# Kernel tuning notes

Measured on AMD Instinct MI355X. Metric: run time of the kernel, lower is better.

## Reference

```python
import jax, jax.numpy as jnp
import numpy as np
import math

C = 91                      # num classes incl. background
BBOX_CLIP = math.log(1000.0 / 16.0)
IMG_H, IMG_W = 800.0, 800.0
SCORE_THRESH = 0.05
NMS_THRESH = 0.5
DETS_PER_IMG = 100
MIN_SIZE = 0.01
WX, WY, WW, WH = 10.0, 10.0, 5.0, 5.0   # bbox_reg_weights


def setup_inputs() -> dict:
    key = jax.random.key(0)
    ks = jax.random.split(key, 8)
    B, N, F_IN, HID = 4, 2048, 12544, 1024
    box_features = jax.random.normal(ks[0], (B, N, F_IN), jnp.float32) * 0.1
    # valid proposal boxes inside an 800x800 image: x1y1 in [0,600], wh in [10,200]
    xy = jax.random.uniform(ks[1], (B, N, 2), jnp.float32, minval=0.0, maxval=600.0)
    wh = jax.random.uniform(ks[2], (B, N, 2), jnp.float32, minval=10.0, maxval=200.0)
    proposals = jnp.concatenate([xy, xy + wh], axis=-1)
    def sc(k, sh, fan):
        return jax.random.normal(k, sh, jnp.float32) * (1.0 / np.sqrt(fan))
    return {
        'box_features': box_features,
        'proposals': proposals,
        'fc6_w': sc(ks[3], (F_IN, HID), F_IN), 'fc6_b': jnp.zeros((HID,), jnp.float32),
        'fc7_w': sc(ks[4], (HID, HID), HID),   'fc7_b': jnp.zeros((HID,), jnp.float32),
        'cls_w': sc(ks[5], (HID, C), HID),     'cls_b': jnp.zeros((C,), jnp.float32),
        'bbox_w': sc(ks[6], (HID, 4 * C), HID), 'bbox_b': jnp.zeros((4 * C,), jnp.float32),
    }


def decode_boxes(rel, props):
    w = props[:, 2] - props[:, 0]
    h = props[:, 3] - props[:, 1]
    cx = props[:, 0] + 0.5 * w
    cy = props[:, 1] + 0.5 * h
    dx = rel[..., 0] / WX
    dy = rel[..., 1] / WY
    dw = jnp.minimum(rel[..., 2] / WW, BBOX_CLIP)
    dh = jnp.minimum(rel[..., 3] / WH, BBOX_CLIP)
    pcx = dx * w[:, None] + cx[:, None]
    pcy = dy * h[:, None] + cy[:, None]
    pw = jnp.exp(dw) * w[:, None]
    ph = jnp.exp(dh) * h[:, None]
    return jnp.stack([pcx - 0.5 * pw, pcy - 0.5 * ph,
                      pcx + 0.5 * pw, pcy + 0.5 * ph], axis=-1)


def postprocess_one(logits, regr, props):
    # logits [N,C], regr [N,4C], props [N,4] -> padded top-DETS_PER_IMG detections
    N = logits.shape[0]
    boxes = decode_boxes(regr.reshape(N, C, 4), props)        # [N,C,4]
    scores = jax.nn.softmax(logits, axis=-1)                  # [N,C]
    # clip_boxes_to_image
    x = jnp.clip(boxes[..., 0::2], 0.0, IMG_W)
    y = jnp.clip(boxes[..., 1::2], 0.0, IMG_H)
    boxes = jnp.stack([x[..., 0], y[..., 0], x[..., 1], y[..., 1]], axis=-1)
    # drop background class, flatten candidates
    boxes = boxes[:, 1:].reshape(-1, 4)                       # [M,4], M=N*(C-1)
    scores = scores[:, 1:].reshape(-1)                        # [M]
    labels = jnp.broadcast_to(jnp.arange(1, C, dtype=jnp.int32)[None, :],
                              (N, C - 1)).reshape(-1)         # [M]
    # score threshold + remove_small_boxes (invalidate instead of dynamic gather)
    bw = boxes[:, 2] - boxes[:, 0]
    bh = boxes[:, 3] - boxes[:, 1]
    valid = (scores > SCORE_THRESH) & (bw >= MIN_SIZE) & (bh >= MIN_SIZE)
    s0 = jnp.where(valid, scores, -jnp.inf)
    # batched_nms via per-class coordinate offset
    offset = labels.astype(boxes.dtype)[:, None] * (max(IMG_H, IMG_W) + 1.0)
    ob = boxes + offset
    area = (ob[:, 2] - ob[:, 0]) * (ob[:, 3] - ob[:, 1])

    def body(sc_cur, _):
        best = jnp.argmax(sc_cur)
        bb = ob[best]
        lt = jnp.maximum(ob[:, :2], bb[:2])
        rb = jnp.minimum(ob[:, 2:], bb[2:])
        inter = jnp.prod(jnp.maximum(rb - lt, 0.0), axis=-1)
        union = jnp.maximum(area + area[best] - inter, 1e-6)
        iou = inter / union
        sc_new = jnp.where(iou > NMS_THRESH, -jnp.inf, sc_cur)
        return sc_new, (best, sc_cur[best])

    _, (keep, kept_s) = jax.lax.scan(body, s0, None, length=DETS_PER_IMG)
    ok = jnp.isfinite(kept_s)
    out_boxes = jnp.where(ok[:, None], boxes[keep], 0.0)      # [D,4]
    out_scores = jnp.where(ok, kept_s, 0.0)                   # [D]
    out_labels = jnp.where(ok, labels[keep], 0)               # [D] int32
    return out_boxes, out_scores, out_labels


def reference(box_features, proposals, fc6_w, fc6_b, fc7_w, fc7_b,
              cls_w, cls_b, bbox_w, bbox_b):
    # TwoMLPHead
    h = jax.nn.relu(box_features @ fc6_w + fc6_b)             # [B,N,1024]
    h = jax.nn.relu(h @ fc7_w + fc7_b)
    # FastRCNNPredictor
    logits = h @ cls_w + cls_b                                # [B,N,C]
    regr = h @ bbox_w + bbox_b                                # [B,N,4C]
    boxes, scores, labels = jax.vmap(postprocess_one)(logits, regr, proposals)
    return boxes, scores, labels
```

## Files before the change

### kernel.cpp

```cpp
#include <hip/hip_runtime.h>
#include <math.h>

#define NIMG   4
#define NPROP  2048
#define MTOT   8192
#define FIN    12544
#define HID    1024
#define NC     91
#define NCB    512
#define DETS   100
#define CAPMAX (NPROP * (NC - 1))
#define VLDS   6144

typedef __attribute__((ext_vector_type(8))) short short8;
typedef __attribute__((ext_vector_type(4))) float f32x4;

__device__ __forceinline__ unsigned short f2bf(float f) {
  union { float f; unsigned u; } v; v.f = f;
  unsigned r = v.u + 0x7fffu + ((v.u >> 16) & 1u);
  return (unsigned short)(r >> 16);
}

__device__ __forceinline__ unsigned cvtpk(float lo, float hi) {
  unsigned r;
  asm("v_cvt_pk_bf16_f32 %0, %1, %2" : "=v"(r) : "v"(lo), "v"(hi));
  return r;
}

__device__ __forceinline__ void gload_lds16(const void* g, void* l) {
  __builtin_amdgcn_global_load_lds((__attribute__((address_space(1))) void*)(g),
                                   (__attribute__((address_space(3))) void*)(l), 16, 0, 0);
}

__global__ void transpose_cvt(const float* __restrict__ in, unsigned short* __restrict__ out,
                              int K, int N, int row_off, int out_ld) {
  __shared__ float tile[32][33];
  int k0 = blockIdx.y * 32, n0 = blockIdx.x * 32;
  int tx = threadIdx.x, ty = threadIdx.y;
#pragma unroll
  for (int i = 0; i < 4; ++i) {
    int r = ty + i * 8;
    if (k0 + r < K && n0 + tx < N)
      tile[r][tx] = in[(size_t)(k0 + r) * N + (n0 + tx)];
  }
  __syncthreads();
#pragma unroll
  for (int i = 0; i < 4; ++i) {
    int r = ty + i * 8;
    if (n0 + r < N && k0 + tx < K)
      out[(size_t)(row_off + n0 + r) * out_ld + (k0 + tx)] = f2bf(tile[tx][r]);
  }
}

__global__ void prep_misc(unsigned short* __restrict__ Wcbt, float* __restrict__ bias_cb,
                          const float* __restrict__ cls_b, const float* __restrict__ bbox_b,
                          int* __restrict__ ccount) {
  int i = blockIdx.x * blockDim.x + threadIdx.x;
  int stride = gridDim.x * blockDim.x;
  for (int j = i; j < 57 * 1024; j += stride) Wcbt[455 * 1024 + j] = 0;
  for (int j = i; j < NCB; j += stride)
    bias_cb[j] = (j < 91) ? cls_b[j] : ((j < 455) ? bbox_b[j - 91] : 0.0f);
  if (i < NIMG) ccount[i] = 0;
}

template <bool AFP32, bool RELU, bool OUTBF16>
__global__ __launch_bounds__(512, 2) void gemm_nt(const void* __restrict__ Av,
                                                  const unsigned short* __restrict__ Bt,
                                                  const float* __restrict__ bias,
                                                  void* __restrict__ Cv,
                                                  int M, int N, int K) {
  __shared__ __align__(16) unsigned short As[2][256 * 64];
  __shared__ __align__(16) unsigned short Bs[2][128 * 64];
  const int tid  = threadIdx.x;
  const int lane = tid & 63;
  const int wid  = tid >> 6;
  const int wm   = (wid >> 1) * 64;
  const int wn   = (wid & 1) * 64;
  const int m0   = blockIdx.x * 256, n0 = blockIdx.y * 128;
  const int lcol = lane & 15;
  const int lk4  = lane >> 4;
  const int rsw  = lcol & 7;

  const int st_r  = lane >> 3;
  const int st_kc = ((lane & 7) ^ st_r) << 3;

  f32x4 acc[4][4];
#pragma unroll
  for (int a = 0; a < 4; ++a)
#pragma unroll
    for (int b = 0; b < 4; ++b)
#pragma unroll
      for (int r = 0; r < 4; ++r) acc[a][b][r] = 0.0f;

  const int NT = K >> 6;
  float4 pa[4][2];

  auto stage_async = [&](int buf, int t) {
    const int k0 = t << 6;
#pragma unroll
    for (int i = 0; i < 2; ++i) {
      int chunk = (wid << 1) | i;
      int r = (chunk << 3) | st_r;
      gload_lds16(Bt + (size_t)(n0 + r) * K + k0 + st_kc, &Bs[buf][chunk << 9]);
    }
    if constexpr (!AFP32) {
#pragma unroll
      for (int i = 0; i < 4; ++i) {
        int chunk = (wid << 2) | i;
        int r = (chunk << 3) | st_r;
        gload_lds16((const unsigned short*)Av + (size_t)(m0 + r) * K + k0 + st_kc,
                    &As[buf][chunk << 9]);
      }
    }
  };
  auto loadA = [&](int t) {
    const int k0 = t << 6;
#pragma unroll
    for (int i = 0; i < 4; ++i) {
      int s = tid + (i << 9);
      int row = s >> 3, kc = (s & 7) << 3;
      const float* gp = (const float*)Av + (size_t)(m0 + row) * K + (k0 + kc);
      pa[i][0] = *(const float4*)gp;
      pa[i][1] = *(const float4*)(gp + 4);
    }
  };
  auto writeA = [&](int buf) {
#pragma unroll
    for (int i = 0; i < 4; ++i) {
      int s = tid + (i << 9);
      int row = s >> 3;
      int slot = ((s & 7) ^ (row & 7)) << 3;
      union { unsigned u32[4]; short8 s8; } pk;
      pk.u32[0] = cvtpk(pa[i][0].x, pa[i][0].y);
      pk.u32[1] = cvtpk(pa[i][0].z, pa[i][0].w);
      pk.u32[2] = cvtpk(pa[i][1].x, pa[i][1].y);
      pk.u32[3] = cvtpk(pa[i][1].z, pa[i][1].w);
      *(short8*)&As[buf][row * 64 + slot] = pk.s8;
    }
  };

  stage_async(0, 0);
  if constexpr (AFP32) { loadA(0); writeA(0); }
  __syncthreads();

  int cur = 0;
  for (int t = 0; t < NT; ++t) {
    const int nxt = cur ^ 1;
    if (t + 1 < NT) {
      stage_async(nxt, t + 1);
      if constexpr (AFP32) loadA(t + 1);
    }
#pragma unroll
    for (int kk = 0; kk < 2; ++kk) {
      const int sb = kk << 2;
      short8 af[4], bf[4];
#pragma unroll
      for (int im = 0; im < 4; ++im)
        af[im] = *(const short8*)&As[cur][(wm + im * 16 + lcol) * 64 + (((sb + lk4) ^ rsw) << 3)];
#pragma unroll
      for (int in = 0; in < 4; ++in)
        bf[in] = *(const short8*)&Bs[cur][(wn + in * 16 + lcol) * 64 + (((sb + lk4) ^ rsw) << 3)];
      __builtin_amdgcn_s_setprio(1);
#pragma unroll
      for (int im = 0; im < 4; ++im)
#pragma unroll
        for (int in = 0; in < 4; ++in)
          acc[im][in] = __builtin_amdgcn_mfma_f32_16x16x32_bf16(af[im], bf[in], acc[im][in], 0, 0, 0);
      __builtin_amdgcn_s_setprio(0);
    }
    if (t + 1 < NT) { if constexpr (AFP32) writeA(nxt); }
    __syncthreads();
    cur = nxt;
  }

  const int r0 = (lane >> 4) * 4;
#pragma unroll
  for (int im = 0; im < 4; ++im) {
#pragma unroll
    for (int in = 0; in < 4; ++in) {
      int gn = n0 + wn + in * 16 + lcol;
      float bv = bias[gn];
#pragma unroll
      for (int r = 0; r < 4; ++r) {
        int gm = m0 + wm + im * 16 + r0 + r;
        float vv = acc[im][in][r] + bv;
        if (RELU) vv = fmaxf(vv, 0.0f);
        if (OUTBF16) ((unsigned short*)Cv)[(size_t)gm * N + gn] = f2bf(vv);
        else         ((float*)Cv)[(size_t)gm * N + gn] = vv;
      }
    }
  }
}

__global__ void candgen(const float* __restrict__ out3, const float* __restrict__ props,
                        float* __restrict__ cscore, float* __restrict__ cbox,
                        int* __restrict__ clabel, int* __restrict__ ccount, int CAP) {
  int gw   = (blockIdx.x * blockDim.x + threadIdx.x) >> 6;
  int lane = threadIdx.x & 63;
  if (gw >= MTOT) return;
  int img = gw >> 11;
  const float* row = out3 + (size_t)gw * NCB;

  float l0 = row[lane];
  float l1 = (lane < NC - 64) ? row[64 + lane] : -INFINITY;
  float mx = fmaxf(l0, l1);
#pragma unroll
  for (int off = 32; off; off >>= 1) mx = fmaxf(mx, __shfl_xor(mx, off));
  float e0 = expf(l0 - mx);
  float e1 = (lane < NC - 64) ? expf(l1 - mx) : 0.0f;
  float den = e0 + e1;
#pragma unroll
  for (int off = 32; off; off >>= 1) den += __shfl_xor(den, off);
  float inv = 1.0f / den;

  float4 p = *(const float4*)(props + (size_t)gw * 4);
  float w = p.z - p.x, h = p.w - p.y;
  float cx = p.x + 0.5f * w, cy = p.y + 0.5f * h;

#pragma unroll
  for (int half = 0; half < 2; ++half) {
    int c = (half << 6) + lane;
    float s = (half ? e1 : e0) * inv;
    if (c >= 1 && c < NC && s > 0.05f) {
      float dx = row[91 + c * 4 + 0] * 0.1f;
      float dy = row[91 + c * 4 + 1] * 0.1f;
      float dw = fminf(row[91 + c * 4 + 2] * 0.2f, 4.135166556742356f);
      float dh = fminf(row[91 + c * 4 + 3] * 0.2f, 4.135166556742356f);
      float pcx = dx * w + cx, pcy = dy * h + cy;
      float pw = expf(dw) * w, ph = expf(dh) * h;
      float x1 = fminf(fmaxf(pcx - 0.5f * pw, 0.0f), 800.0f);
      float x2 = fminf(fmaxf(pcx + 0.5f * pw, 0.0f), 800.0f);
      float y1 = fminf(fmaxf(pcy - 0.5f * ph, 0.0f), 800.0f);
      float y2 = fminf(fmaxf(pcy + 0.5f * ph, 0.0f), 800.0f);
      if (x2 - x1 >= 0.01f && y2 - y1 >= 0.01f) {
        int idx = atomicAdd(&ccount[img], 1);
        if (idx < CAP) {
          size_t o = (size_t)img * CAP + idx;
          cscore[o] = s;
          clabel[o] = c;
          cbox[o * 4 + 0] = x1; cbox[o * 4 + 1] = y1;
          cbox[o * 4 + 2] = x2; cbox[o * 4 + 3] = y2;
        }
      }
    }
  }
}

__global__ __launch_bounds__(1024) void nms_kernel(float* __restrict__ cscore, const float* __restrict__ cbox,
                           const int* __restrict__ clabel, const int* __restrict__ ccount,
                           float* __restrict__ out, int CAP) {
  int img = blockIdx.x;
  int tid = threadIdx.x;
  int lane = tid & 63, wid = tid >> 6;
  int V = ccount[img]; if (V > CAP) V = CAP;
  int VL = V < VLDS ? V : VLDS;
  float* sc = cscore + (size_t)img * CAP;
  const float* bx = cbox + (size_t)img * CAP * 4;
  const int* lb = clabel + (size_t)img * CAP;
  float* ob  = out + (size_t)img * DETS * 4;
  float* osd = out + (size_t)NIMG * DETS * 4 + (size_t)img * DETS;
  float* ol  = out + (size_t)NIMG * DETS * 5 + (size_t)img * DETS;

  for (int t = tid; t < DETS; t += blockDim.x) {
    ob[t * 4 + 0] = 0.0f; ob[t * 4 + 1] = 0.0f; ob[t * 4 + 2] = 0.0f; ob[t * 4 + 3] = 0.0f;
    osd[t] = 0.0f; ol[t] = 0.0f;
  }

  __shared__ float sx1[VLDS], sy1[VLDS], sx2[VLDS], sy2[VLDS], sar[VLDS], ssc[VLDS];
  __shared__ float rs[16]; __shared__ int ri[16];
  __shared__ float bbs[6];
  __shared__ int   bbest;

  for (int t = tid; t < VL; t += blockDim.x) {
    float4 b = *(const float4*)&bx[(size_t)t * 4];
    float offv = (float)lb[t] * 801.0f;
    sx1[t] = b.x + offv; sy1[t] = b.y + offv;
    sx2[t] = b.z + offv; sy2[t] = b.w + offv;
    sar[t] = (b.z - b.x) * (b.w - b.y);
    ssc[t] = sc[t];
  }
  __syncthreads();

  for (int d = 0; d < DETS; ++d) {
    float bs = -INFINITY; int bi = -1;
    for (int t = tid; t < VL; t += blockDim.x) { float v = ssc[t]; if (v > bs) { bs = v; bi = t; } }
    if (V > VLDS)
      for (int t = VLDS + tid; t < V; t += blockDim.x) { float v = sc[t]; if (v > bs) { bs = v; bi = t; } }
#pragma unroll
    for (int off = 32; off; off >>= 1) {
      float osf = __shfl_xor(bs, off); int oi = __shfl_xor(bi, off);
      if (osf > bs) { bs = osf; bi = oi; }
    }
    if (lane == 0) { rs[wid] = bs; ri[wid] = bi; }
    __syncthreads();
    if (tid == 0) {
      float b0 = rs[0]; int i0 = ri[0];
      for (int wv = 1; wv < 16; ++wv) if (rs[wv] > b0) { b0 = rs[wv]; i0 = ri[wv]; }
      if (i0 < 0 || !(b0 > -INFINITY)) {
        bbest = -1;
      } else {
        bbest = i0;
        float ox1, oy1, ox2, oy2, ar;
        if (i0 < VLDS) { ox1 = sx1[i0]; oy1 = sy1[i0]; ox2 = sx2[i0]; oy2 = sy2[i0]; ar = sar[i0]; }
        else {
          float4 b = *(const float4*)&bx[(size_t)i0 * 4];
          float offv = (float)lb[i0] * 801.0f;
          ox1 = b.x + offv; oy1 = b.y + offv; ox2 = b.z + offv; oy2 = b.w + offv;
          ar = (b.z - b.x) * (b.w - b.y);
        }
        bbs[0] = ox1; bbs[1] = oy1; bbs[2] = ox2; bbs[3] = oy2; bbs[4] = ar;
        float4 rb = *(const float4*)&bx[(size_t)i0 * 4];
        ob[d * 4 + 0] = rb.x; ob[d * 4 + 1] = rb.y; ob[d * 4 + 2] = rb.z; ob[d * 4 + 3] = rb.w;
        osd[d] = b0;
        ol[d] = (float)lb[i0];
      }
    }
    __syncthreads();
    if (bbest < 0) break;
    float bx1 = bbs[0], by1 = bbs[1], bx2 = bbs[2], by2 = bbs[3], barea = bbs[4];
    for (int t = tid; t < VL; t += blockDim.x) {
      float ltx = fmaxf(sx1[t], bx1), lty = fmaxf(sy1[t], by1);
      float rbx = fminf(sx2[t], bx2), rby = fminf(sy2[t], by2);
      float inter = fmaxf(rbx - ltx, 0.0f) * fmaxf(rby - lty, 0.0f);
      float uni = fmaxf(sar[t] + barea - inter, 1e-6f);
      if (inter / uni > 0.5f) ssc[t] = -INFINITY;
    }
    if (V > VLDS) {
      for (int t = VLDS + tid; t < V; t += blockDim.x) {
        float4 b = *(const float4*)&bx[(size_t)t * 4];
        float offv = (float)lb[t] * 801.0f;
        float tx1 = b.x + offv, ty1 = b.y + offv, tx2 = b.z + offv, ty2 = b.w + offv;
        float ltx = fmaxf(tx1, bx1), lty = fmaxf(ty1, by1);
        float rbx = fminf(tx2, bx2), rby = fminf(ty2, by2);
        float inter = fmaxf(rbx - ltx, 0.0f) * fmaxf(rby - lty, 0.0f);
        float areat = (tx2 - tx1) * (ty2 - ty1);
        float uni = fmaxf(areat + barea - inter, 1e-6f);
        if (inter / uni > 0.5f) sc[t] = -INFINITY;
      }
    }
    __syncthreads();
  }
}

extern "C" void kernel_launch(void* const* d_in, const int* in_sizes, int n_in,
                              void* d_out, int out_size, void* d_ws, size_t ws_size,
                              hipStream_t stream) {
  const float* box_features = (const float*)d_in[0];
  const float* proposals    = (const float*)d_in[1];
  const float* fc6_w = (const float*)d_in[2];
  const float* fc6_b = (const float*)d_in[3];
  const float* fc7_w = (const float*)d_in[4];
  const float* fc7_b = (const float*)d_in[5];
  const float* cls_w = (const float*)d_in[6];
  const float* cls_b = (const float*)d_in[7];
  const float* bbox_w = (const float*)d_in[8];
  const float* bbox_b = (const float*)d_in[9];

  char* ws = (char*)d_ws;
  size_t off = 0;
  unsigned short* W6t  = (unsigned short*)(ws + off); off += (size_t)HID * FIN * 2;
  unsigned short* W7t  = (unsigned short*)(ws + off); off += (size_t)HID * HID * 2;
  unsigned short* Wcbt = (unsigned short*)(ws + off); off += (size_t)NCB * HID * 2;
  float* bias_cb       = (float*)(ws + off);          off += (size_t)NCB * 4;
  int*   ccount        = (int*)(ws + off);            off += 256;
  unsigned short* h1   = (unsigned short*)(ws + off); off += (size_t)MTOT * HID * 2;
  unsigned short* h2   = (unsigned short*)(ws + off); off += (size_t)MTOT * HID * 2;
  float* out3          = (float*)(ws + off);          off += (size_t)MTOT * NCB * 4;

  int CAP = CAPMAX;
  if (ws_size > off) {
    size_t avail = ws_size - off;
    size_t cap_ws = avail / 96;
    if (cap_ws < (size_t)CAP) CAP = (int)cap_ws;
  } else {
    CAP = 0;
  }
  float* cscore = (float*)(ws + off);
  int*   clabel = (int*)(ws + off + (size_t)NIMG * CAP * 4);
  float* cbox   = (float*)(ws + off + (size_t)NIMG * CAP * 8);

  transpose_cvt<<<dim3(HID / 32, FIN / 32), dim3(32, 8), 0, stream>>>(fc6_w, W6t, FIN, HID, 0, FIN);
  transpose_cvt<<<dim3(HID / 32, HID / 32), dim3(32, 8), 0, stream>>>(fc7_w, W7t, HID, HID, 0, HID);
  transpose_cvt<<<dim3(3,  HID / 32), dim3(32, 8), 0, stream>>>(cls_w,  Wcbt, HID, 91,  0,  HID);
  transpose_cvt<<<dim3(12, HID / 32), dim3(32, 8), 0, stream>>>(bbox_w, Wcbt, HID, 364, 91, HID);
  prep_misc<<<64, 256, 0, stream>>>(Wcbt, bias_cb, cls_b, bbox_b, ccount);

  gemm_nt<true,  true,  true ><<<dim3(MTOT / 256, HID / 128), 512, 0, stream>>>(
      box_features, W6t, fc6_b, h1, MTOT, HID, FIN);
  gemm_nt<false, true,  true ><<<dim3(MTOT / 256, HID / 128), 512, 0, stream>>>(
      h1, W7t, fc7_b, h2, MTOT, HID, HID);
  gemm_nt<false, false, false><<<dim3(MTOT / 256, NCB / 128), 512, 0, stream>>>(
      h2, Wcbt, bias_cb, out3, MTOT, NCB, HID);

  candgen<<<(MTOT * 64) / 256, 256, 0, stream>>>(out3, proposals, cscore, cbox, clabel, ccount, CAP);
  nms_kernel<<<NIMG, 1024, 0, stream>>>(cscore, cbox, clabel, ccount, (float*)d_out, CAP);
}
```

Measured before the change: 991.7 us.

## Reshape GEMM tiles to 128x256 and hand-tune vmcnt waits for prefetch overlap

Each GEMM block now covers 128 rows and 256 columns (128 for the final small GEMM) instead of 256x128. The large fp32 activation matrix in fc6 is therefore re-read across half as many column tiles, which cuts global traffic on the dominant operand. The loop also replaces __syncthreads with explicit s_waitcnt vmcnt counts and raw barriers. This lets the next tile's loads stay in flight while the current tile is computed. In exchange there are fewer accumulators per wave along M, and occupancy and LDS use change. The hand-counted vmcnt values must match the number of loads issued, or correctness breaks.

```diff
diff --git a/kernel.cpp b/kernel.cpp
--- a/kernel.cpp
+++ b/kernel.cpp
@@ -32,6 +32,13 @@
                                    (__attribute__((address_space(3))) void*)(l), 16, 0, 0);
 }
 
+template <int N> __device__ __forceinline__ void waitcnt_vm() {
+  if constexpr (N == 8)      asm volatile("s_waitcnt vmcnt(8)" ::: "memory");
+  else if constexpr (N == 6) asm volatile("s_waitcnt vmcnt(6)" ::: "memory");
+  else if constexpr (N == 4) asm volatile("s_waitcnt vmcnt(4)" ::: "memory");
+  else                       asm volatile("s_waitcnt vmcnt(0)" ::: "memory");
+}
+
 __global__ void transpose_cvt(const float* __restrict__ in, unsigned short* __restrict__ out,
                               int K, int N, int row_off, int out_ld) {
   __shared__ float tile[32][33];
@@ -63,20 +70,24 @@
   if (i < NIMG) ccount[i] = 0;
 }
 
-template <bool AFP32, bool RELU, bool OUTBF16>
-__global__ __launch_bounds__(512, 2) void gemm_nt(const void* __restrict__ Av,
-                                                  const unsigned short* __restrict__ Bt,
-                                                  const float* __restrict__ bias,
-                                                  void* __restrict__ Cv,
-                                                  int M, int N, int K) {
-  __shared__ __align__(16) unsigned short As[2][256 * 64];
-  __shared__ __align__(16) unsigned short Bs[2][128 * 64];
+template <int BN, bool AFP32, bool RELU, bool OUTBF16>
+__global__ __launch_bounds__(512, (BN == 256) ? 2 : 4)
+void gemm_nt(const void* __restrict__ Av, const unsigned short* __restrict__ Bt,
+             const float* __restrict__ bias, void* __restrict__ Cv,
+             int M, int N, int K) {
+  constexpr int WN   = BN / 4;
+  constexpr int NAN_ = WN / 16;
+  constexpr int BCH  = BN / 64;
+  constexpr int VISS = AFP32 ? 8 : (2 + BCH);
+
+  __shared__ __align__(16) unsigned short As[2][128 * 64];
+  __shared__ __align__(16) unsigned short Bs[2][BN * 64];
   const int tid  = threadIdx.x;
   const int lane = tid & 63;
   const int wid  = tid >> 6;
-  const int wm   = (wid >> 1) * 64;
-  const int wn   = (wid & 1) * 64;
-  const int m0   = blockIdx.x * 256, n0 = blockIdx.y * 128;
+  const int wm   = (wid >> 2) * 64;
+  const int wn   = (wid & 3) * WN;
+  const int m0   = blockIdx.x * 128, n0 = blockIdx.y * BN;
   const int lcol = lane & 15;
   const int lk4  = lane >> 4;
   const int rsw  = lcol & 7;
@@ -84,29 +95,29 @@
   const int st_r  = lane >> 3;
   const int st_kc = ((lane & 7) ^ st_r) << 3;
 
-  f32x4 acc[4][4];
+  f32x4 acc[4][NAN_];
 #pragma unroll
   for (int a = 0; a < 4; ++a)
 #pragma unroll
-    for (int b = 0; b < 4; ++b)
+    for (int b = 0; b < NAN_; ++b)
 #pragma unroll
       for (int r = 0; r < 4; ++r) acc[a][b][r] = 0.0f;
 
   const int NT = K >> 6;
-  float4 pa[4][2];
+  float4 pa[2][2];
 
   auto stage_async = [&](int buf, int t) {
     const int k0 = t << 6;
 #pragma unroll
-    for (int i = 0; i < 2; ++i) {
-      int chunk = (wid << 1) | i;
+    for (int i = 0; i < BCH; ++i) {
+      int chunk = wid * BCH + i;
       int r = (chunk << 3) | st_r;
       gload_lds16(Bt + (size_t)(n0 + r) * K + k0 + st_kc, &Bs[buf][chunk << 9]);
     }
     if constexpr (!AFP32) {
 #pragma unroll
-      for (int i = 0; i < 4; ++i) {
-        int chunk = (wid << 2) | i;
+      for (int i = 0; i < 2; ++i) {
+        int chunk = (wid << 1) | i;
         int r = (chunk << 3) | st_r;
         gload_lds16((const unsigned short*)Av + (size_t)(m0 + r) * K + k0 + st_kc,
                     &As[buf][chunk << 9]);
@@ -116,7 +127,7 @@
   auto loadA = [&](int t) {
     const int k0 = t << 6;
 #pragma unroll
-    for (int i = 0; i < 4; ++i) {
+    for (int i = 0; i < 2; ++i) {
       int s = tid + (i << 9);
       int row = s >> 3, kc = (s & 7) << 3;
       const float* gp = (const float*)Av + (size_t)(m0 + row) * K + (k0 + kc);
@@ -126,7 +137,7 @@
   };
   auto writeA = [&](int buf) {
 #pragma unroll
-    for (int i = 0; i < 4; ++i) {
+    for (int i = 0; i < 2; ++i) {
       int s = tid + (i << 9);
       int row = s >> 3;
       int slot = ((s & 7) ^ (row & 7)) << 3;
@@ -139,37 +150,52 @@
     }
   };
 
+  if constexpr (AFP32) loadA(0);
   stage_async(0, 0);
-  if constexpr (AFP32) { loadA(0); writeA(0); }
-  __syncthreads();
+  if constexpr (AFP32) writeA(0);
+  asm volatile("s_waitcnt vmcnt(0) lgkmcnt(0)" ::: "memory");
+  __builtin_amdgcn_s_barrier();
+  __builtin_amdgcn_sched_barrier(0);
 
   int cur = 0;
   for (int t = 0; t < NT; ++t) {
     const int nxt = cur ^ 1;
     if (t + 1 < NT) {
+      if constexpr (AFP32) loadA(t + 1);
       stage_async(nxt, t + 1);
-      if constexpr (AFP32) loadA(t + 1);
-    }
+      waitcnt_vm<VISS>();
+    } else {
+      waitcnt_vm<0>();
+    }
+    __builtin_amdgcn_s_barrier();
+    __builtin_amdgcn_sched_barrier(0);
 #pragma unroll
     for (int kk = 0; kk < 2; ++kk) {
       const int sb = kk << 2;
-      short8 af[4], bf[4];
+      short8 af[4], bf[NAN_];
 #pragma unroll
       for (int im = 0; im < 4; ++im)
         af[im] = *(const short8*)&As[cur][(wm + im * 16 + lcol) * 64 + (((sb + lk4) ^ rsw) << 3)];
 #pragma unroll
-      for (int in = 0; in < 4; ++in)
+      for (int in = 0; in < NAN_; ++in)
         bf[in] = *(const short8*)&Bs[cur][(wn + in * 16 + lcol) * 64 + (((sb + lk4) ^ rsw) << 3)];
       __builtin_amdgcn_s_setprio(1);
 #pragma unroll
       for (int im = 0; im < 4; ++im)
 #pragma unroll
-        for (int in = 0; in < 4; ++in)
+        for (int in = 0; in < NAN_; ++in)
           acc[im][in] = __builtin_amdgcn_mfma_f32_16x16x32_bf16(af[im], bf[in], acc[im][in], 0, 0, 0);
       __builtin_amdgcn_s_setprio(0);
     }
-    if (t + 1 < NT) { if constexpr (AFP32) writeA(nxt); }
-    __syncthreads();
+    if (t + 1 < NT) {
+      if constexpr (AFP32) {
+        writeA(nxt);
+        asm volatile("s_waitcnt lgkmcnt(0)" ::: "memory");
+      }
+    }
+    __builtin_amdgcn_sched_barrier(0);
+    __builtin_amdgcn_s_barrier();
+    __builtin_amdgcn_sched_barrier(0);
     cur = nxt;
   }
 
@@ -177,7 +203,7 @@
 #pragma unroll
   for (int im = 0; im < 4; ++im) {
 #pragma unroll
-    for (int in = 0; in < 4; ++in) {
+    for (int in = 0; in < NAN_; ++in) {
       int gn = n0 + wn + in * 16 + lcol;
       float bv = bias[gn];
 #pragma unroll
@@ -385,11 +411,11 @@
   transpose_cvt<<<dim3(12, HID / 32), dim3(32, 8), 0, stream>>>(bbox_w, Wcbt, HID, 364, 91, HID);
   prep_misc<<<64, 256, 0, stream>>>(Wcbt, bias_cb, cls_b, bbox_b, ccount);
 
-  gemm_nt<true,  true,  true ><<<dim3(MTOT / 256, HID / 128), 512, 0, stream>>>(
+  gemm_nt<256, true,  true,  true ><<<dim3(MTOT / 128, HID / 256), 512, 0, stream>>>(
       box_features, W6t, fc6_b, h1, MTOT, HID, FIN);
-  gemm_nt<false, true,  true ><<<dim3(MTOT / 256, HID / 128), 512, 0, stream>>>(
+  gemm_nt<256, false, true,  true ><<<dim3(MTOT / 128, HID / 256), 512, 0, stream>>>(
       h1, W7t, fc7_b, h2, MTOT, HID, HID);
-  gemm_nt<false, false, false><<<dim3(MTOT / 256, NCB / 128), 512, 0, stream>>>(
+  gemm_nt<128, false, false, false><<<dim3(MTOT / 128, NCB / 128), 512, 0, stream>>>(
       h2, Wcbt, bias_cb, out3, MTOT, NCB, HID);
 
   candgen<<<(MTOT * 64) / 256, 256, 0, stream>>>(out3, proposals, cscore, cbox, clabel, ccount, CAP);
```

Result: faster. 937.0 us (-5.5%).
